# Performance work log

Hardware: AMD Instinct MI355X
Metric: run time of the kernel (lower is better)

## Reference

```python
import jax, jax.numpy as jnp
import numpy as np

B, T, D_IN = 8192, 12, 64   # trajectories, traj length (== max_length), input dim
HID, ENC, R = 512, 128, 64  # encoder hidden, encoded_dim, MPS rank
OUT = 1


def _uniform(key, shape, bound):
    return jax.random.uniform(key, shape, jnp.float32, -bound, bound)


def setup_inputs() -> dict:
    key = jax.random.key(0)
    ks = jax.random.split(key, 8)
    x = jax.random.normal(ks[0], (B, T, D_IN), jnp.float32)
    # encoder Linear params (Kaiming-uniform-like scale)
    W1 = _uniform(ks[1], (HID, D_IN), 1.0 / np.sqrt(D_IN))
    b1 = _uniform(ks[2], (HID,), 1.0 / np.sqrt(D_IN))
    W2 = _uniform(ks[3], (ENC, HID), 1.0 / np.sqrt(HID))
    b2 = _uniform(ks[4], (ENC,), 1.0 / np.sqrt(HID))
    # MPS cores with if_rescale_weights bound = 1/sqrt(prod(dims))
    H_first = _uniform(ks[5], (1, ENC, R), 1.0 / np.sqrt(1 * ENC * R))
    H_mid = _uniform(ks[6], (T - 2, R, ENC, R), 1.0 / np.sqrt(R * ENC * R))
    H_last = _uniform(ks[7], (R, ENC, OUT), 1.0 / np.sqrt(R * ENC * OUT))
    return {"x": x, "W1": W1, "b1": b1, "W2": W2, "b2": b2,
            "H_first": H_first, "H_mid": H_mid, "H_last": H_last}


def reference(x, W1, b1, W2, b2, H_first, H_mid, H_last):
    Bn, Tn, _ = x.shape
    # two-layer encoder MLP with ReLU after each layer
    h = jax.nn.relu(jnp.einsum('btd,hd->bth', x, W1) + b1)
    enc = jax.nn.relu(jnp.einsum('bth,eh->bte', h, W2) + b2)  # [B, T, ENC]
    # contract each timestep's encoding with its core along the physical dim
    v = jnp.einsum('be,oer->br', enc[:, 0], H_first)              # [B, R] (dim0==1 squeezed)
    M = jnp.einsum('bte,tper->btpr', enc[:, 1:Tn - 1], H_mid)     # [B, T-2, R, R]
    # sequential chain product (vector-matrix, associative scan structure)
    for t in range(Tn - 2):
        v = jnp.einsum('bp,bpr->br', v, M[:, t])
    last = jnp.einsum('be,per->bpr', enc[:, -1], H_last)          # [B, R, OUT]
    out = jnp.einsum('bp,bpo->bo', v, last)                       # [B, OUT]
    return out.squeeze(-1)                                        # [B] (output_dim == 1)
```

## Files before the change

### kernel.cpp

```cpp
#include <hip/hip_runtime.h>
#include <hip/hip_fp16.h>


#define B_ALL 8192
#define TT    12

typedef short bfrag __attribute__((ext_vector_type(8)));
typedef _Float16 hfrag __attribute__((ext_vector_type(8)));
typedef float ffrag __attribute__((ext_vector_type(16)));

#define O_ENC   0ULL
#define O_HMH   25165824ULL
#define O_HML   35651584ULL
#define O_W1F   46137344ULL
#define O_W2F   46202880ULL
#define O_VBUF  46333952ULL

__device__ __forceinline__ unsigned short bf16_rne(float f) {
    unsigned int u = __builtin_bit_cast(unsigned int, f);
    unsigned int r = (u + 0x7fffu + ((u >> 16) & 1u)) >> 16;
    return (unsigned short)r;
}
__device__ __forceinline__ float bf16_f32(unsigned short h) {
    unsigned int u = ((unsigned int)h) << 16;
    return __builtin_bit_cast(float, u);
}

__device__ __forceinline__ void st_f1_sc1(float* p, float v) {
    __hip_atomic_store(p, v, __ATOMIC_RELAXED, __HIP_MEMORY_SCOPE_AGENT);
}
__device__ __forceinline__ float2 ld_f2_sc1(const float* p) {
    unsigned long long u = __hip_atomic_load((unsigned long long*)(size_t)p,
                                             __ATOMIC_RELAXED,
                                             __HIP_MEMORY_SCOPE_AGENT);
    return __builtin_bit_cast(float2, u);
}

__global__ __launch_bounds__(256)
void prep_kernel(const float* __restrict__ W1, const float* __restrict__ W2,
                 const float* __restrict__ Hm,
                 __half* __restrict__ w1f, __half* __restrict__ w2f,
                 unsigned short* __restrict__ Hh, unsigned short* __restrict__ Hl)
{
    const int tid = threadIdx.x;
    const int bid = blockIdx.x;
    if (bid < 1280) {
        __shared__ unsigned short hs[4096], ls[4096];
        const int t = bid >> 7, e = bid & 127;
        const float* src = Hm + ((size_t)t * 64 * 128 + e) * 64;
        const int p  = tid >> 2;
        const int rc = (tid & 3) * 16;
        const int fp = (p >> 4) * 512 + ((p >> 3) & 1) * 256 + (p & 7);
        #pragma unroll
        for (int k4 = 0; k4 < 4; ++k4) {
            const int r0 = rc + k4 * 4;
            const float4 v4 = *(const float4*)&src[(size_t)p * 8192 + r0];
            const float vv[4] = {v4.x, v4.y, v4.z, v4.w};
            #pragma unroll
            for (int k = 0; k < 4; ++k) {
                const int r = r0 + k;
                const int f = (r >> 5) * 2048 + (r & 31) * 8 + fp;
                const float val = vv[k];
                const unsigned short hi = bf16_rne(val);
                const unsigned short lo = bf16_rne(val - bf16_f32(hi));
                hs[f] = hi;
                ls[f] = lo;
            }
        }
        __syncthreads();
        const size_t q0 = (size_t)t * 524288 + (size_t)e * 4096 + tid * 16;
        *(uint4*)&Hh[q0]     = *(const uint4*)&hs[tid * 16];
        *(uint4*)&Hh[q0 + 8] = *(const uint4*)&hs[tid * 16 + 8];
        *(uint4*)&Hl[q0]     = *(const uint4*)&ls[tid * 16];
        *(uint4*)&Hl[q0 + 8] = *(const uint4*)&ls[tid * 16 + 8];
    } else {
        const int wb = bid - 1280;
        const long long N_W1 = 32768, N_W2 = 65536;
        for (long long idx = wb * 256 + tid; idx < N_W1 + N_W2; idx += 8 * 256) {
            if (idx < N_W1) {
                const int w = (int)idx;
                const int jn = w >> 11, ks = (w >> 9) & 3, half = (w >> 8) & 1;
                const int jl = (w >> 3) & 31, jj = w & 7;
                const int j = jn * 32 + jl, d = ks * 16 + half * 8 + jj;
                w1f[w] = __float2half(W1[j * 64 + d]);
            } else {
                const int w = (int)(idx - N_W1);
                const int en = w >> 14, ks2g = (w >> 9) & 31, half = (w >> 8) & 1;
                const int el = (w >> 3) & 31, jj = w & 7;
                const int e = en * 32 + el, j = ks2g * 16 + half * 8 + jj;
                w2f[w] = __float2half(W2[e * 512 + j]);
            }
        }
    }
}

__global__ __launch_bounds__(256)
void enc_kernel(const float* __restrict__ x,
                const float* __restrict__ b1, const float* __restrict__ b2,
                const __half* __restrict__ w1f, const __half* __restrict__ w2f,
                __half* __restrict__ encH)
{
    __shared__ __align__(16) unsigned char smem[17408];
    float* x_s  = (float*)smem;
    __half* h_s = (__half*)smem;

    const int tid   = threadIdx.x;
    const int wv    = tid >> 6;
    const int lane  = tid & 63;
    const int l32   = lane & 31;
    const int half  = lane >> 5;
    const int msub  = wv >> 1;
    const int nhalf = wv & 1;
    const int m0    = blockIdx.x * 64;

    #pragma unroll
    for (int i = 0; i < 4; ++i) {
        const int f4 = i * 256 + tid;
        const int r = f4 >> 4, c4 = (f4 & 15) * 4;
        *(float4*)&x_s[r * 68 + c4] =
            *(const float4*)&x[(long long)(m0 + r) * 64 + c4];
    }
    __syncthreads();

    hfrag xa[4];
    #pragma unroll
    for (int ks = 0; ks < 4; ++ks) {
        const float* src = &x_s[(msub * 32 + l32) * 68 + ks * 16 + half * 8];
        const float4 a = *(const float4*)src;
        const float4 b = *(const float4*)(src + 4);
        hfrag v;
        v[0] = (_Float16)a.x; v[1] = (_Float16)a.y;
        v[2] = (_Float16)a.z; v[3] = (_Float16)a.w;
        v[4] = (_Float16)b.x; v[5] = (_Float16)b.y;
        v[6] = (_Float16)b.z; v[7] = (_Float16)b.w;
        xa[ks] = v;
    }
    __syncthreads();

    ffrag c2[2];
    c2[0] = 0.0f; c2[1] = 0.0f;

    for (int chunk = 0; chunk < 4; ++chunk) {
        ffrag c1[2];
        float b1j[2];
        #pragma unroll
        for (int nf = 0; nf < 2; ++nf) {
            const int jn = chunk * 4 + nhalf * 2 + nf;
            b1j[nf] = b1[jn * 32 + l32];
            ffrag acc = 0.0f;
            #pragma unroll
            for (int ks = 0; ks < 4; ++ks) {
                const hfrag bh = *(const hfrag*)(w1f + (jn * 4 + ks) * 512
                                                 + half * 256 + l32 * 8);
                acc = __builtin_amdgcn_mfma_f32_32x32x16_f16(xa[ks], bh, acc, 0, 0, 0);
            }
            c1[nf] = acc;
        }
        __syncthreads();
        #pragma unroll
        for (int nf = 0; nf < 2; ++nf) {
            #pragma unroll
            for (int i2 = 0; i2 < 16; ++i2) {
                const int m_row = (i2 & 3) + 8 * (i2 >> 2) + 4 * half;
                const float v = fmaxf(c1[nf][i2] + b1j[nf], 0.0f);
                h_s[(msub * 32 + m_row) * 136 + nhalf * 64 + nf * 32 + l32] =
                    __float2half(v);
            }
        }
        __syncthreads();
        #pragma unroll
        for (int ks2 = 0; ks2 < 8; ++ks2) {
            const hfrag a = *(const hfrag*)&h_s[(msub * 32 + l32) * 136
                                                + ks2 * 16 + half * 8];
            const int ks2g = chunk * 8 + ks2;
            #pragma unroll
            for (int ef = 0; ef < 2; ++ef) {
                const int en = nhalf * 2 + ef;
                const hfrag b = *(const hfrag*)(w2f + (en * 32 + ks2g) * 512
                                                + half * 256 + l32 * 8);
                c2[ef] = __builtin_amdgcn_mfma_f32_32x32x16_f16(a, b, c2[ef], 0, 0, 0);
            }
        }
    }

    #pragma unroll
    for (int ef = 0; ef < 2; ++ef) {
        const int e = nhalf * 64 + ef * 32 + l32;
        const float b2e = b2[e];
        #pragma unroll
        for (int i2 = 0; i2 < 16; ++i2) {
            const int m_row = (i2 & 3) + 8 * (i2 >> 2) + 4 * half;
            const int m_g = m0 + msub * 32 + m_row;
            encH[(long long)m_g * 128 + e] =
                __float2half(fmaxf(c2[ef][i2] + b2e, 0.0f));
        }
    }
}

__device__ unsigned int g_flag[256 * 32];

__global__ __launch_bounds__(512, 1)
void chain_all(const unsigned short* __restrict__ HmH,
               const unsigned short* __restrict__ HmL,
               const __half* __restrict__ encH,
               const float* __restrict__ Hf,
               const float* __restrict__ HL,
               float* vbuf,
               float* __restrict__ out)
{
    __shared__ __align__(16) unsigned char smem[52800];
    float* vsum  = (float*)smem;
    float* enc_s = (float*)(smem + 16896);
    float* red   = (float*)(smem + 50688);

    const int tid  = threadIdx.x;
    const int bid  = blockIdx.x;
    const int pid  = bid >> 1;
    const int rr   = bid & 1;
    const int b0   = pid * 64;
    const int lane = tid & 63;
    const int wv   = tid >> 6;
    const int l32  = lane & 31;
    const int half = lane >> 5;
    const int eq   = wv >> 1;
    const int bh   = wv & 1;
    const int bcol = bh * 32 + l32;

    unsigned int fbase = 0;
    if (tid == 0)
        fbase = __hip_atomic_load(&g_flag[bid * 32], __ATOMIC_RELAXED,
                                  __HIP_MEMORY_SCOPE_AGENT);

    const int sbL = tid >> 3;
    const int seo = (tid & 7) * 16;
    #define STAGE_ENC(T)                                                        \
    {                                                                           \
        const __half* er_ = encH + ((size_t)(b0 + sbL) * 12 + (T)) * 128 + seo; \
        uint4 u0_ = *(const uint4*)er_;                                         \
        uint4 u1_ = *(const uint4*)(er_ + 8);                                   \
        const __half* hp_ = (const __half*)&u0_;                                \
        const __half* hq_ = (const __half*)&u1_;                                \
        _Pragma("unroll")                                                       \
        for (int j = 0; j < 8; ++j)                                             \
            enc_s[(seo + j) * 66 + sbL] = __half2float(hp_[j]);                 \
        _Pragma("unroll")                                                       \
        for (int j = 0; j < 8; ++j)                                             \
            enc_s[(seo + 8 + j) * 66 + sbL] = __half2float(hq_[j]);             \
    }

    {
        STAGE_ENC(0);
        __syncthreads();
        const int pg = tid >> 6, bI = tid & 63;
        float acc[8] = {0, 0, 0, 0, 0, 0, 0, 0};
        for (int e = 0; e < 128; ++e) {
            const float ev = enc_s[e * 66 + bI];
            const float4 h0 = *(const float4*)&Hf[e * 64 + pg * 8];
            const float4 h1 = *(const float4*)&Hf[e * 64 + pg * 8 + 4];
            acc[0] += ev * h0.x; acc[1] += ev * h0.y;
            acc[2] += ev * h0.z; acc[3] += ev * h0.w;
            acc[4] += ev * h1.x; acc[5] += ev * h1.y;
            acc[6] += ev * h1.z; acc[7] += ev * h1.w;
        }
        #pragma unroll
        for (int i = 0; i < 8; ++i)
            vsum[(pg * 8 + i) * 66 + bI] = acc[i];
        __syncthreads();
    }

    const unsigned short* Hsh = HmH;
    const unsigned short* Hsl = HmL;
    const int lanoff = rr * 2048 + half * 256 + l32 * 8;

    #pragma unroll 1
    for (int t = 1; t <= 10; ++t) {
        STAGE_ENC(t);

        bfrag vbh_[4], vbl_[4];
        #pragma unroll
        for (int s = 0; s < 4; ++s) {
            const int p0 = s * 16 + half * 8;
            bfrag hb, lb;
            #pragma unroll
            for (int j = 0; j < 8; ++j) {
                const float f = vsum[(p0 + j) * 66 + bcol];
                const unsigned short hi = bf16_rne(f);
                const unsigned short lo = bf16_rne(f - bf16_f32(hi));
                hb[j] = (short)hi;
                lb[j] = (short)lo;
            }
            vbh_[s] = hb;
            vbl_[s] = lb;
        }
        __syncthreads();

        const unsigned short* hp = Hsh + (size_t)(eq * 32) * 4096 + lanoff;
        const unsigned short* lp = Hsl + (size_t)(eq * 32) * 4096 + lanoff;
        bfrag cah[4], cal[4];
        #pragma unroll
        for (int s = 0; s < 4; ++s) {
            cah[s] = *(const bfrag*)(hp + s * 512);
            cal[s] = *(const bfrag*)(lp + s * 512);
        }
        ffrag z = 0.0f;
        ffrag vn = 0.0f;
        #pragma unroll 2
        for (int e = 0; e < 32; ++e) {
            hp += 4096; lp += 4096;
            bfrag nah[4], nal[4];
            #pragma unroll
            for (int s = 0; s < 4; ++s) {
                nah[s] = *(const bfrag*)(hp + s * 512);
                nal[s] = *(const bfrag*)(lp + s * 512);
            }
            const float ev = enc_s[(eq * 32 + e) * 66 + bcol];
            ffrag w = z;
            #pragma unroll
            for (int s = 0; s < 4; ++s) {
                w = __builtin_amdgcn_mfma_f32_32x32x16_bf16(cah[s], vbh_[s], w, 0, 0, 0);
                w = __builtin_amdgcn_mfma_f32_32x32x16_bf16(cah[s], vbl_[s], w, 0, 0, 0);
                w = __builtin_amdgcn_mfma_f32_32x32x16_bf16(cal[s], vbh_[s], w, 0, 0, 0);
            }
            vn += w * ev;
            #pragma unroll
            for (int s = 0; s < 4; ++s) { cah[s] = nah[s]; cal[s] = nal[s]; }
        }
        __syncthreads();

        float4* sc4 = (float4*)enc_s;
        if (eq != 0) {
            const int slot = (eq - 1) * 2 + bh;
            #pragma unroll
            for (int q = 0; q < 4; ++q) {
                float4 f4 = {vn[q * 4 + 0], vn[q * 4 + 1],
                             vn[q * 4 + 2], vn[q * 4 + 3]};
                sc4[(slot * 4 + q) * 66 + lane] = f4;
            }
        }
        __syncthreads();
        if (eq == 0) {
            #pragma unroll
            for (int g = 1; g < 4; ++g) {
                const int slot = (g - 1) * 2 + bh;
                #pragma unroll
                for (int q = 0; q < 4; ++q) {
                    const float4 f4 = sc4[(slot * 4 + q) * 66 + lane];
                    vn[q * 4 + 0] += f4.x; vn[q * 4 + 1] += f4.y;
                    vn[q * 4 + 2] += f4.z; vn[q * 4 + 3] += f4.w;
                }
            }
            float* vb = vbuf + (((size_t)pid * 2 + (t & 1)) * 2 + rr) * 2048;
            #pragma unroll
            for (int i = 0; i < 16; ++i) {
                const int roffs = (i & 3) + 8 * (i >> 2) + 4 * half;
                vsum[(rr * 32 + roffs) * 66 + bcol] = vn[i];
                st_f1_sc1(&vb[roffs * 64 + bcol], vn[i]);
            }
        }
        __syncthreads();

        if (tid == 0) {
            __hip_atomic_store(&g_flag[bid * 32], fbase + t, __ATOMIC_RELAXED,
                               __HIP_MEMORY_SCOPE_AGENT);
            while (__hip_atomic_load(&g_flag[(bid ^ 1) * 32], __ATOMIC_RELAXED,
                                     __HIP_MEMORY_SCOPE_AGENT) < fbase + t)
                __builtin_amdgcn_s_sleep(8);
        }
        __syncthreads();

        {
            const float* pb = vbuf + (((size_t)pid * 2 + (t & 1)) * 2 + (rr ^ 1)) * 2048;
            const int i4 = tid * 4;
            const int r_l = i4 >> 6, bc = i4 & 63;
            const float2 u0 = ld_f2_sc1(pb + i4);
            const float2 u1 = ld_f2_sc1(pb + i4 + 2);
            float* dst = &vsum[((rr ^ 1) * 32 + r_l) * 66 + bc];
            dst[0] = u0.x; dst[1] = u0.y; dst[2] = u1.x; dst[3] = u1.y;
        }
        __syncthreads();

        Hsh += 524288;
        Hsl += 524288;
    }

    {
        STAGE_ENC(11);
        __syncthreads();
        const int pg = tid >> 6, bI = tid & 63;
        float s = 0.0f;
        #pragma unroll
        for (int i = 0; i < 8; ++i) {
            const int p = pg * 8 + i;
            float L = 0.0f;
            #pragma unroll 16
            for (int e = 0; e < 128; ++e)
                L += enc_s[e * 66 + bI] * HL[p * 128 + e];
            s += vsum[p * 66 + bI] * L;
        }
        red[pg * 66 + bI] = s;
        __syncthreads();
        if (rr == 0 && tid < 64) {
            float acc = 0.0f;
            #pragma unroll
            for (int g = 0; g < 8; ++g)
                acc += red[g * 66 + tid];
            out[b0 + tid] = acc;
        }
    }
    #undef STAGE_ENC
}

extern "C" void kernel_launch(void* const* d_in, const int* in_sizes, int n_in,
                              void* d_out, int out_size, void* d_ws, size_t ws_size,
                              hipStream_t stream) {
    const float* x  = (const float*)d_in[0];
    const float* W1 = (const float*)d_in[1];
    const float* b1 = (const float*)d_in[2];
    const float* W2 = (const float*)d_in[3];
    const float* b2 = (const float*)d_in[4];
    const float* Hf = (const float*)d_in[5];
    const float* Hm = (const float*)d_in[6];
    const float* HL = (const float*)d_in[7];
    float* out = (float*)d_out;
    (void)in_sizes; (void)n_in; (void)out_size; (void)ws_size;

    char* ws = (char*)d_ws;
    __half* encH        = (__half*)(ws + O_ENC);
    unsigned short* HmH = (unsigned short*)(ws + O_HMH);
    unsigned short* HmL = (unsigned short*)(ws + O_HML);
    __half* w1f         = (__half*)(ws + O_W1F);
    __half* w2f         = (__half*)(ws + O_W2F);
    float* vbuf         = (float*)(ws + O_VBUF);

    prep_kernel<<<dim3(1288), dim3(256), 0, stream>>>(W1, W2, Hm, w1f, w2f, HmH, HmL);
    enc_kernel<<<dim3(1536), dim3(256), 0, stream>>>(x, b1, b2, w1f, w2f, encH);
    chain_all<<<dim3(256), dim3(512), 0, stream>>>(HmH, HmL, encH, Hf, HL, vbuf, out);
}
```

Baseline: 446.4 us.

## Merge block pairs into one block per batch tile, drop inter-block flag sync

Previously two blocks cooperated on each 64-trajectory tile, each computing half of the R output rows and exchanging partial vectors through global memory with spin-wait flags every timestep. Now a single 512-thread block computes both row halves: each wave handles both batch halves with two accumulator chains, and the result goes straight into shared memory. This removes the global round-trip and spin-wait latency per step. In exchange it halves the grid to 128 blocks, so fewer CUs are busy, and each wave carries more register state.

```diff
diff --git a/kernel.cpp b/kernel.cpp
--- a/kernel.cpp
+++ b/kernel.cpp
@@ -4,6 +4,8 @@
 
 #define B_ALL 8192
 #define TT    12
+#define B_T   64
+#define NBLK  128
 
 typedef short bfrag __attribute__((ext_vector_type(8)));
 typedef _Float16 hfrag __attribute__((ext_vector_type(8)));
@@ -14,7 +16,6 @@
 #define O_HML   35651584ULL
 #define O_W1F   46137344ULL
 #define O_W2F   46202880ULL
-#define O_VBUF  46333952ULL
 
 __device__ __forceinline__ unsigned short bf16_rne(float f) {
     unsigned int u = __builtin_bit_cast(unsigned int, f);
@@ -24,16 +25,6 @@
 __device__ __forceinline__ float bf16_f32(unsigned short h) {
     unsigned int u = ((unsigned int)h) << 16;
     return __builtin_bit_cast(float, u);
-}
-
-__device__ __forceinline__ void st_f1_sc1(float* p, float v) {
-    __hip_atomic_store(p, v, __ATOMIC_RELAXED, __HIP_MEMORY_SCOPE_AGENT);
-}
-__device__ __forceinline__ float2 ld_f2_sc1(const float* p) {
-    unsigned long long u = __hip_atomic_load((unsigned long long*)(size_t)p,
-                                             __ATOMIC_RELAXED,
-                                             __HIP_MEMORY_SCOPE_AGENT);
-    return __builtin_bit_cast(float2, u);
 }
 
 __global__ __launch_bounds__(256)
@@ -197,15 +188,12 @@
     }
 }
 
-__device__ unsigned int g_flag[256 * 32];
-
 __global__ __launch_bounds__(512, 1)
 void chain_all(const unsigned short* __restrict__ HmH,
                const unsigned short* __restrict__ HmL,
                const __half* __restrict__ encH,
                const float* __restrict__ Hf,
                const float* __restrict__ HL,
-               float* vbuf,
                float* __restrict__ out)
 {
     __shared__ __align__(16) unsigned char smem[52800];
@@ -214,22 +202,13 @@
     float* red   = (float*)(smem + 50688);
 
     const int tid  = threadIdx.x;
-    const int bid  = blockIdx.x;
-    const int pid  = bid >> 1;
-    const int rr   = bid & 1;
-    const int b0   = pid * 64;
+    const int b0   = blockIdx.x * B_T;
     const int lane = tid & 63;
     const int wv   = tid >> 6;
     const int l32  = lane & 31;
     const int half = lane >> 5;
     const int eq   = wv >> 1;
-    const int bh   = wv & 1;
-    const int bcol = bh * 32 + l32;
-
-    unsigned int fbase = 0;
-    if (tid == 0)
-        fbase = __hip_atomic_load(&g_flag[bid * 32], __ATOMIC_RELAXED,
-                                  __HIP_MEMORY_SCOPE_AGENT);
+    const int rh   = wv & 1;
 
     const int sbL = tid >> 3;
     const int seo = (tid & 7) * 16;
@@ -270,27 +249,30 @@
 
     const unsigned short* Hsh = HmH;
     const unsigned short* Hsl = HmL;
-    const int lanoff = rr * 2048 + half * 256 + l32 * 8;
+    const int lanoff = rh * 2048 + half * 256 + l32 * 8;
 
     #pragma unroll 1
     for (int t = 1; t <= 10; ++t) {
         STAGE_ENC(t);
 
-        bfrag vbh_[4], vbl_[4];
-        #pragma unroll
-        for (int s = 0; s < 4; ++s) {
-            const int p0 = s * 16 + half * 8;
-            bfrag hb, lb;
-            #pragma unroll
-            for (int j = 0; j < 8; ++j) {
-                const float f = vsum[(p0 + j) * 66 + bcol];
-                const unsigned short hi = bf16_rne(f);
-                const unsigned short lo = bf16_rne(f - bf16_f32(hi));
-                hb[j] = (short)hi;
-                lb[j] = (short)lo;
-            }
-            vbh_[s] = hb;
-            vbl_[s] = lb;
+        bfrag vbh[2][4], vbl[2][4];
+        #pragma unroll
+        for (int bh = 0; bh < 2; ++bh) {
+            #pragma unroll
+            for (int s = 0; s < 4; ++s) {
+                const int p0 = s * 16 + half * 8;
+                bfrag hb, lb;
+                #pragma unroll
+                for (int j = 0; j < 8; ++j) {
+                    const float f = vsum[(p0 + j) * 66 + bh * 32 + l32];
+                    const unsigned short hi = bf16_rne(f);
+                    const unsigned short lo = bf16_rne(f - bf16_f32(hi));
+                    hb[j] = (short)hi;
+                    lb[j] = (short)lo;
+                }
+                vbh[bh][s] = hb;
+                vbl[bh][s] = lb;
+            }
         }
         __syncthreads();
 
@@ -303,7 +285,7 @@
             cal[s] = *(const bfrag*)(lp + s * 512);
         }
         ffrag z = 0.0f;
-        ffrag vn = 0.0f;
+        ffrag vn0 = 0.0f, vn1 = 0.0f;
         #pragma unroll 2
         for (int e = 0; e < 32; ++e) {
             hp += 4096; lp += 4096;
@@ -313,69 +295,60 @@
                 nah[s] = *(const bfrag*)(hp + s * 512);
                 nal[s] = *(const bfrag*)(lp + s * 512);
             }
-            const float ev = enc_s[(eq * 32 + e) * 66 + bcol];
-            ffrag w = z;
+            const float ev0 = enc_s[(eq * 32 + e) * 66 + l32];
+            const float ev1 = enc_s[(eq * 32 + e) * 66 + 32 + l32];
+            ffrag w0 = z, w1 = z;
             #pragma unroll
             for (int s = 0; s < 4; ++s) {
-                w = __builtin_amdgcn_mfma_f32_32x32x16_bf16(cah[s], vbh_[s], w, 0, 0, 0);
-                w = __builtin_amdgcn_mfma_f32_32x32x16_bf16(cah[s], vbl_[s], w, 0, 0, 0);
-                w = __builtin_amdgcn_mfma_f32_32x32x16_bf16(cal[s], vbh_[s], w, 0, 0, 0);
-            }
-            vn += w * ev;
+                w0 = __builtin_amdgcn_mfma_f32_32x32x16_bf16(cah[s], vbh[0][s], w0, 0, 0, 0);
+                w1 = __builtin_amdgcn_mfma_f32_32x32x16_bf16(cah[s], vbh[1][s], w1, 0, 0, 0);
+                w0 = __builtin_amdgcn_mfma_f32_32x32x16_bf16(cah[s], vbl[0][s], w0, 0, 0, 0);
+                w1 = __builtin_amdgcn_mfma_f32_32x32x16_bf16(cah[s], vbl[1][s], w1, 0, 0, 0);
+                w0 = __builtin_amdgcn_mfma_f32_32x32x16_bf16(cal[s], vbh[0][s], w0, 0, 0, 0);
+                w1 = __builtin_amdgcn_mfma_f32_32x32x16_bf16(cal[s], vbh[1][s], w1, 0, 0, 0);
+            }
+            vn0 += w0 * ev0;
+            vn1 += w1 * ev1;
             #pragma unroll
             for (int s = 0; s < 4; ++s) { cah[s] = nah[s]; cal[s] = nal[s]; }
         }
         __syncthreads();
 
-        float4* sc4 = (float4*)enc_s;
+        float4* sc4 = (float4*)smem;
         if (eq != 0) {
-            const int slot = (eq - 1) * 2 + bh;
-            #pragma unroll
-            for (int q = 0; q < 4; ++q) {
-                float4 f4 = {vn[q * 4 + 0], vn[q * 4 + 1],
-                             vn[q * 4 + 2], vn[q * 4 + 3]};
-                sc4[(slot * 4 + q) * 66 + lane] = f4;
-            }
-        }
-        __syncthreads();
-        if (eq == 0) {
-            #pragma unroll
-            for (int g = 1; g < 4; ++g) {
-                const int slot = (g - 1) * 2 + bh;
+            #pragma unroll
+            for (int bh = 0; bh < 2; ++bh) {
+                const ffrag vv = bh ? vn1 : vn0;
+                const int slot = (eq - 1) * 4 + rh * 2 + bh;
                 #pragma unroll
                 for (int q = 0; q < 4; ++q) {
-                    const float4 f4 = sc4[(slot * 4 + q) * 66 + lane];
-                    vn[q * 4 + 0] += f4.x; vn[q * 4 + 1] += f4.y;
-                    vn[q * 4 + 2] += f4.z; vn[q * 4 + 3] += f4.w;
+                    float4 f4 = {vv[q * 4 + 0], vv[q * 4 + 1],
+                                 vv[q * 4 + 2], vv[q * 4 + 3]};
+                    sc4[(slot * 4 + q) * 66 + lane] = f4;
                 }
             }
-            float* vb = vbuf + (((size_t)pid * 2 + (t & 1)) * 2 + rr) * 2048;
+        }
+        __syncthreads();
+        if (eq == 0) {
+            #pragma unroll
+            for (int g = 1; g < 4; ++g) {
+                const int s0 = (g - 1) * 4 + rh * 2;
+                #pragma unroll
+                for (int q = 0; q < 4; ++q) {
+                    const float4 f0 = sc4[(s0 * 4 + q) * 66 + lane];
+                    const float4 f1 = sc4[((s0 + 1) * 4 + q) * 66 + lane];
+                    vn0[q * 4 + 0] += f0.x; vn0[q * 4 + 1] += f0.y;
+                    vn0[q * 4 + 2] += f0.z; vn0[q * 4 + 3] += f0.w;
+                    vn1[q * 4 + 0] += f1.x; vn1[q * 4 + 1] += f1.y;
+                    vn1[q * 4 + 2] += f1.z; vn1[q * 4 + 3] += f1.w;
+                }
+            }
             #pragma unroll
             for (int i = 0; i < 16; ++i) {
-                const int roffs = (i & 3) + 8 * (i >> 2) + 4 * half;
-                vsum[(rr * 32 + roffs) * 66 + bcol] = vn[i];
-                st_f1_sc1(&vb[roffs * 64 + bcol], vn[i]);
-            }
-        }
-        __syncthreads();
-
-        if (tid == 0) {
-            __hip_atomic_store(&g_flag[bid * 32], fbase + t, __ATOMIC_RELAXED,
-                               __HIP_MEMORY_SCOPE_AGENT);
-            while (__hip_atomic_load(&g_flag[(bid ^ 1) * 32], __ATOMIC_RELAXED,
-                                     __HIP_MEMORY_SCOPE_AGENT) < fbase + t)
-                __builtin_amdgcn_s_sleep(8);
-        }
-        __syncthreads();
-
-        {
-            const float* pb = vbuf + (((size_t)pid * 2 + (t & 1)) * 2 + (rr ^ 1)) * 2048;
-            const int i4 = tid * 4;
-            const int r_l = i4 >> 6, bc = i4 & 63;
-            const float2 u0 = ld_f2_sc1(pb + i4);
-            const float2 u1 = ld_f2_sc1(pb + i4 + 2);
-            float* dst = &vsum[((rr ^ 1) * 32 + r_l) * 66 + bc];
-            dst[0] = u0.x; dst[1] = u0.y; dst[2] = u1.x; dst[3] = u1.y;
+                const int r = rh * 32 + (i & 3) + 8 * (i >> 2) + 4 * half;
+                vsum[r * 66 + l32]      = vn0[i];
+                vsum[r * 66 + 32 + l32] = vn1[i];
+            }
         }
         __syncthreads();
 
@@ -399,7 +372,7 @@
         }
         red[pg * 66 + bI] = s;
         __syncthreads();
-        if (rr == 0 && tid < 64) {
+        if (tid < 64) {
             float acc = 0.0f;
             #pragma unroll
             for (int g = 0; g < 8; ++g)
@@ -430,9 +403,8 @@
     unsigned short* HmL = (unsigned short*)(ws + O_HML);
     __half* w1f         = (__half*)(ws + O_W1F);
     __half* w2f         = (__half*)(ws + O_W2F);
-    float* vbuf         = (float*)(ws + O_VBUF);
 
     prep_kernel<<<dim3(1288), dim3(256), 0, stream>>>(W1, W2, Hm, w1f, w2f, HmH, HmL);
     enc_kernel<<<dim3(1536), dim3(256), 0, stream>>>(x, b1, b2, w1f, w2f, encH);
-    chain_all<<<dim3(256), dim3(512), 0, stream>>>(HmH, HmL, encH, Hf, HL, vbuf, out);
-}
+    chain_all<<<dim3(NBLK), dim3(512), 0, stream>>>(HmH, HmL, encH, Hf, HL, out);
+}
```

New measurement: 504.5 us. +13.0%, slower.
